# Kernel tuning notes

Measured on AMD Instinct MI355X. Metric: run time of the kernel, lower is better.

Reference implementation:

```python
import jax, jax.numpy as jnp
import numpy as np

INPUT_SIZE = 768
HIDDEN = 384


def _gru_dir(x, W_ih, W_hh, b_ih, b_hh, reverse):
    """Single-direction GRU, torch gate order (r, z, n).
    x: [B, S, D] -> outputs [B, S, H]."""
    B = x.shape[0]
    H = W_hh.shape[1]
    # Precompute input projections for all timesteps: [B, S, 3H] -> [S, B, 3H]
    xw = jnp.swapaxes(x @ W_ih.T + b_ih, 0, 1)

    def step(h, xw_t):
        gh = h @ W_hh.T + b_hh
        xr, xz, xn = jnp.split(xw_t, 3, axis=-1)
        hr, hz, hn = jnp.split(gh, 3, axis=-1)
        r = jax.nn.sigmoid(xr + hr)
        z = jax.nn.sigmoid(xz + hz)
        n = jnp.tanh(xn + r * hn)
        h_new = (1.0 - z) * n + z * h
        return h_new, h_new

    h0 = jnp.zeros((B, H), dtype=x.dtype)
    _, hs = jax.lax.scan(step, h0, xw, reverse=reverse)  # [S, B, H]
    return jnp.swapaxes(hs, 0, 1)


def setup_inputs() -> dict:
    key = jax.random.key(0)
    ks = jax.random.split(key, 12)
    B, S, D, H = 32, 512, INPUT_SIZE, HIDDEN
    s_ih = 1.0 / np.sqrt(H)
    u = lambda k, shape: jax.random.uniform(k, shape, jnp.float32, -s_ih, s_ih)
    inp = {
        "ip": jax.random.normal(ks[0], (B, S, D), jnp.float32),
        # forward-direction GRU params
        "W_ih_f": u(ks[1], (3 * H, D)),
        "W_hh_f": u(ks[2], (3 * H, H)),
        "b_ih_f": u(ks[3], (3 * H,)),
        "b_hh_f": u(ks[4], (3 * H,)),
        # backward-direction GRU params
        "W_ih_b": u(ks[5], (3 * H, D)),
        "W_hh_b": u(ks[6], (3 * H, H)),
        "b_ih_b": u(ks[7], (3 * H,)),
        "b_hh_b": u(ks[8], (3 * H,)),
        # sentence attention params (input_dim = 2H)
        "W_attn": u(ks[9], (2 * H, 2 * H)),
        "b_attn": u(ks[10], (2 * H,)),
        "context": jax.random.normal(ks[11], (2 * H,), jnp.float32) * 0.05,
    }
    return inp


def reference(ip, W_ih_f, W_hh_f, b_ih_f, b_hh_f,
              W_ih_b, W_hh_b, b_ih_b, b_hh_b,
              W_attn, b_attn, context):
    # BiGRU encode: concat forward & backward hidden states -> [B, S, 2H]
    h_f = _gru_dir(ip, W_ih_f, W_hh_f, b_ih_f, b_hh_f, reverse=False)
    h_b = _gru_dir(ip, W_ih_b, W_hh_b, b_ih_b, b_hh_b, reverse=True)
    out = jnp.concatenate([h_f, h_b], axis=-1)
    # Additive attention pooling over sentences
    scores = jnp.tanh(out @ W_attn.T + b_attn) @ context  # [B, S]
    attn = jax.nn.softmax(scores, axis=1)
    doc_embeds = jnp.einsum("bs,bsd->bd", attn, out)  # [B, 2H]
    return doc_embeds
```

## Files before the change

kernel.cpp:

```cpp
#include <hip/hip_runtime.h>
#include <hip/hip_fp16.h>

typedef _Float16 half2_t __attribute__((ext_vector_type(2)));
typedef _Float16 half4_t __attribute__((ext_vector_type(4)));
typedef _Float16 half8_t __attribute__((ext_vector_type(8)));
typedef float floatx4 __attribute__((ext_vector_type(4)));

#define B_   32
#define S_   512
#define D_   768
#define H_   384
#define H3_  1152
#define M_   (B_*S_)
#define N2_  (2*H3_)
#define TWOH_ 768
#define NWG_DIR 6
#define JSPAN 64

__device__ __forceinline__ void load16_cc3(const void* p0, const void* p1, const void* p2,
                                           int4& v0, int4& v1, int4& v2) {
  unsigned long long a0 = (unsigned long long)p0;
  unsigned long long a1 = (unsigned long long)p1;
  unsigned long long a2 = (unsigned long long)p2;
  asm volatile("global_load_dwordx4 %0, %3, off sc1\n\t"
               "global_load_dwordx4 %1, %4, off sc1\n\t"
               "global_load_dwordx4 %2, %5, off sc1\n\t"
               "s_waitcnt vmcnt(0)"
               : "=&v"(v0), "=&v"(v1), "=&v"(v2)
               : "v"(a0), "v"(a1), "v"(a2) : "memory");
}
__device__ __forceinline__ void store8_cc(void* p, int2 v) {
  unsigned long long a = (unsigned long long)p;
  asm volatile("global_store_dwordx2 %0, %1, off sc1" :: "v"(a), "v"(v) : "memory");
}
__device__ __forceinline__ void wait_vm0() {
  asm volatile("s_waitcnt vmcnt(0)" ::: "memory");
}

__global__ void cvt_f32_f16_kernel(const float* __restrict__ src,
                                   _Float16* __restrict__ dst, int n4) {
  int i = blockIdx.x * blockDim.x + threadIdx.x;
  if (i >= n4) return;
  float4 v = ((const float4*)src)[i];
  half4_t h = {(_Float16)v.x, (_Float16)v.y, (_Float16)v.z, (_Float16)v.w};
  ((half4_t*)dst)[i] = h;
}

__global__ __launch_bounds__(256) void gemm_xw_kernel(
    const _Float16* __restrict__ A, const _Float16* __restrict__ Bm,
    const float* __restrict__ bias_f, const float* __restrict__ bias_b,
    _Float16* __restrict__ xw) {
  __shared__ _Float16 As[64][40];
  __shared__ _Float16 Bs[64][40];
  const int m0 = blockIdx.x * 64, n0 = blockIdx.y * 64;
  const int tid = threadIdx.x, lane = tid & 63, w = tid >> 6;
  const int wm = w >> 1, wn = w & 1;
  const int q = lane >> 4, c = lane & 15;
  floatx4 acc[2][2] = {};

  const int t = tid & 127;
  const int srow = t >> 1, skh = (t & 1) * 16;
  const _Float16* gsrc =
      (tid < 128 ? A + (size_t)(m0 + srow) * D_ : Bm + (size_t)(n0 + srow) * D_) + skh;
  _Float16* ldst = (tid < 128) ? &As[srow][skh] : &Bs[srow][skh];

  for (int k0 = 0; k0 < D_; k0 += 32) {
    half8_t v0 = *(const half8_t*)(gsrc + k0);
    half8_t v1 = *(const half8_t*)(gsrc + k0 + 8);
    __syncthreads();
    *(half8_t*)ldst = v0;
    *(half8_t*)(ldst + 8) = v1;
    __syncthreads();
    half8_t a0 = *(const half8_t*)&As[wm * 32 + c][q * 8];
    half8_t a1 = *(const half8_t*)&As[wm * 32 + 16 + c][q * 8];
    half8_t b0 = *(const half8_t*)&Bs[wn * 32 + c][q * 8];
    half8_t b1 = *(const half8_t*)&Bs[wn * 32 + 16 + c][q * 8];
    acc[0][0] = __builtin_amdgcn_mfma_f32_16x16x32_f16(a0, b0, acc[0][0], 0, 0, 0);
    acc[0][1] = __builtin_amdgcn_mfma_f32_16x16x32_f16(a0, b1, acc[0][1], 0, 0, 0);
    acc[1][0] = __builtin_amdgcn_mfma_f32_16x16x32_f16(a1, b0, acc[1][0], 0, 0, 0);
    acc[1][1] = __builtin_amdgcn_mfma_f32_16x16x32_f16(a1, b1, acc[1][1], 0, 0, 0);
  }
  for (int mi = 0; mi < 2; ++mi)
    for (int ni = 0; ni < 2; ++ni)
      for (int r = 0; r < 4; ++r) {
        int m = m0 + wm * 32 + mi * 16 + q * 4 + r;
        int n = n0 + wn * 32 + ni * 16 + c;
        int dir = n >= H3_;
        int nn = n - dir * H3_;
        float bv = dir ? bias_b[nn] : bias_f[nn];
        float vv = acc[mi][ni][r] + bv;
        int s = m & (S_ - 1), bb = m >> 9;
        xw[(((size_t)dir * S_ + s) * B_ + bb) * H3_ + nn] = (_Float16)vv;
      }
}

__global__ __launch_bounds__(512, 2) void gru_mfma_kernel(
    const _Float16* __restrict__ xw,
    const _Float16* __restrict__ Whh,
    const float* __restrict__ bhh_f, const float* __restrict__ bhh_b,
    _Float16* __restrict__ hglob,
    _Float16* __restrict__ out16,
    int* __restrict__ bar) {
  const int wg = blockIdx.x;
  const int dir = wg / NWG_DIR;
  const int wgj = wg % NWG_DIR;
  const int j0w = wgj * JSPAN;
  const int tid = threadIdx.x, lane = tid & 63, w = tid >> 6;
  const int bt = w & 1, jt = w >> 1;
  const int c = lane & 15, q = lane >> 4;

  __shared__ __align__(16) _Float16 hS[32 * 392];

  half8_t bfr[3][12];
  {
    const int jglob = j0w + jt * 16 + c;
#pragma unroll
    for (int g = 0; g < 3; ++g) {
      const _Float16* wp = Whh + ((size_t)dir * H3_ + g * H_ + jglob) * H_ + q * 8;
#pragma unroll
      for (int kt = 0; kt < 12; ++kt) bfr[g][kt] = *(const half8_t*)(wp + kt * 32);
    }
  }
  const float* bhh = dir ? bhh_b : bhh_f;
  const int bl = bt * 16 + c;
  const int jg4 = j0w + jt * 16 + q * 4;
  const float4 br4 = *(const float4*)&bhh[jg4];
  const float4 bz4 = *(const float4*)&bhh[H_ + jg4];
  const float4 bn4 = *(const float4*)&bhh[2 * H_ + jg4];
  float hc[4] = {0.f, 0.f, 0.f, 0.f};

  int* flg = bar + dir * 256;

  for (int step = 0; step < S_; ++step) {
    const int t = dir ? (S_ - 1 - step) : step;
    const int par = step & 1;

    const _Float16* xbase = xw + (((size_t)dir * S_ + t) * B_ + bl) * H3_ + jg4;
    half4_t xr4 = *(const half4_t*)(xbase);
    half4_t xz4 = *(const half4_t*)(xbase + H_);
    half4_t xn4 = *(const half4_t*)(xbase + 2 * H_);

    if (step > 0 && w == 0) {
      int v;
      do {
        v = (lane < NWG_DIR)
                ? __hip_atomic_load(&flg[lane * 16], __ATOMIC_RELAXED,
                                    __HIP_MEMORY_SCOPE_AGENT)
                : 0x7fffffff;
      } while (!__all(v >= step));
    }
    __syncthreads();

    {
      const _Float16* hb = hglob + ((size_t)dir * 2 + par) * B_ * H_;
      int g0 = tid, g1 = tid + 512, g2 = tid + 1024;
      int4 v0, v1, v2;
      load16_cc3(hb + (g0 / 48) * H_ + (g0 % 48) * 8,
                 hb + (g1 / 48) * H_ + (g1 % 48) * 8,
                 hb + (g2 / 48) * H_ + (g2 % 48) * 8, v0, v1, v2);
      *(int4*)&hS[(g0 / 48) * 392 + (g0 % 48) * 8] = v0;
      *(int4*)&hS[(g1 / 48) * 392 + (g1 % 48) * 8] = v1;
      *(int4*)&hS[(g2 / 48) * 392 + (g2 % 48) * 8] = v2;
    }
    __syncthreads();

    floatx4 a0 = {}, a1 = {}, a2 = {};
    {
      const _Float16* hrow = &hS[(bt * 16 + c) * 392 + q * 8];
#pragma unroll
      for (int kt = 0; kt < 12; ++kt) {
        half8_t hf = *(const half8_t*)(hrow + kt * 32);
        a0 = __builtin_amdgcn_mfma_f32_16x16x32_f16(bfr[0][kt], hf, a0, 0, 0, 0);
        a1 = __builtin_amdgcn_mfma_f32_16x16x32_f16(bfr[1][kt], hf, a1, 0, 0, 0);
        a2 = __builtin_amdgcn_mfma_f32_16x16x32_f16(bfr[2][kt], hf, a2, 0, 0, 0);
      }
    }

    half4_t hh;
#pragma unroll
    for (int r = 0; r < 4; ++r) {
      float rr = 1.f / (1.f + __expf(-((float)xr4[r] + a0[r] + br4[r])));
      float zz = 1.f / (1.f + __expf(-((float)xz4[r] + a1[r] + bz4[r])));
      float u = (float)xn4[r] + rr * (a2[r] + bn4[r]);
      float e = __expf(-2.f * u);
      float nv = (1.f - e) / (1.f + e);
      hc[r] = (1.f - zz) * nv + zz * hc[r];
      hh[r] = (_Float16)hc[r];
    }
    store8_cc(hglob + (((size_t)dir * 2 + (par ^ 1)) * B_ + bl) * H_ + jg4,
              __builtin_bit_cast(int2, hh));
    wait_vm0();
    __syncthreads();
    if (tid == 0)
      __hip_atomic_store(&flg[wgj * 16], step + 1, __ATOMIC_RELAXED,
                         __HIP_MEMORY_SCOPE_AGENT);
    *(half4_t*)&out16[((size_t)bl * S_ + t) * TWOH_ + dir * H_ + jg4] = hh;
  }
}

__global__ __launch_bounds__(256) void attn_score_kernel(
    const _Float16* __restrict__ A ,
    const _Float16* __restrict__ Bm ,
    const float* __restrict__ b_attn, const float* __restrict__ ctx,
    float* __restrict__ scores) {
  __shared__ _Float16 As[64][40];
  __shared__ _Float16 Bs[64][40];
  const int m0 = blockIdx.x * 64, n0 = blockIdx.y * 64;
  const int tid = threadIdx.x, lane = tid & 63, w = tid >> 6;
  const int wm = w >> 1, wn = w & 1;
  const int q = lane >> 4, c = lane & 15;
  floatx4 acc[2][2] = {};

  const int t = tid & 127;
  const int srow = t >> 1, skh = (t & 1) * 16;
  const _Float16* gsrc =
      (tid < 128 ? A + (size_t)(m0 + srow) * D_ : Bm + (size_t)(n0 + srow) * D_) + skh;
  _Float16* ldst = (tid < 128) ? &As[srow][skh] : &Bs[srow][skh];

  for (int k0 = 0; k0 < D_; k0 += 32) {
    half8_t v0 = *(const half8_t*)(gsrc + k0);
    half8_t v1 = *(const half8_t*)(gsrc + k0 + 8);
    __syncthreads();
    *(half8_t*)ldst = v0;
    *(half8_t*)(ldst + 8) = v1;
    __syncthreads();
    half8_t a0 = *(const half8_t*)&As[wm * 32 + c][q * 8];
    half8_t a1 = *(const half8_t*)&As[wm * 32 + 16 + c][q * 8];
    half8_t b0 = *(const half8_t*)&Bs[wn * 32 + c][q * 8];
    half8_t b1 = *(const half8_t*)&Bs[wn * 32 + 16 + c][q * 8];
    acc[0][0] = __builtin_amdgcn_mfma_f32_16x16x32_f16(a0, b0, acc[0][0], 0, 0, 0);
    acc[0][1] = __builtin_amdgcn_mfma_f32_16x16x32_f16(a0, b1, acc[0][1], 0, 0, 0);
    acc[1][0] = __builtin_amdgcn_mfma_f32_16x16x32_f16(a1, b0, acc[1][0], 0, 0, 0);
    acc[1][1] = __builtin_amdgcn_mfma_f32_16x16x32_f16(a1, b1, acc[1][1], 0, 0, 0);
  }
  for (int mi = 0; mi < 2; ++mi)
    for (int ni = 0; ni < 2; ++ni)
      for (int r = 0; r < 4; ++r) {
        int n = n0 + wn * 32 + ni * 16 + c;
        float vv = tanhf(acc[mi][ni][r] + b_attn[n]) * ctx[n];
        vv += __shfl_xor(vv, 1);
        vv += __shfl_xor(vv, 2);
        vv += __shfl_xor(vv, 4);
        vv += __shfl_xor(vv, 8);
        if (c == 0) {
          int m = m0 + wm * 32 + mi * 16 + q * 4 + r;
          atomicAdd(&scores[m], vv);
        }
      }
}

__global__ __launch_bounds__(256) void softmax_kernel(const float* __restrict__ scores,
                                                      float* __restrict__ attn) {
  const int b = blockIdx.x, tid = threadIdx.x;
  __shared__ float red[8];
  float s0 = scores[b * S_ + tid], s1 = scores[b * S_ + 256 + tid];
  float m = fmaxf(s0, s1);
  for (int off = 1; off < 64; off <<= 1) m = fmaxf(m, __shfl_xor(m, off));
  int wv = tid >> 6;
  if ((tid & 63) == 0) red[wv] = m;
  __syncthreads();
  m = fmaxf(fmaxf(red[0], red[1]), fmaxf(red[2], red[3]));
  float e0 = expf(s0 - m), e1 = expf(s1 - m);
  float sum = e0 + e1;
  for (int off = 1; off < 64; off <<= 1) sum += __shfl_xor(sum, off);
  if ((tid & 63) == 0) red[4 + wv] = sum;
  __syncthreads();
  sum = red[4] + red[5] + red[6] + red[7];
  float inv = 1.0f / sum;
  attn[b * S_ + tid] = e0 * inv;
  attn[b * S_ + 256 + tid] = e1 * inv;
}

__global__ __launch_bounds__(384) void doc_kernel(const float* __restrict__ attn,
                                                  const _Float16* __restrict__ out16,
                                                  float* __restrict__ dout) {
  const int b = blockIdx.x, tid = threadIdx.x;
  __shared__ float at[S_];
  for (int i = tid; i < S_; i += 384) at[i] = attn[b * S_ + i];
  __syncthreads();
  const half2_t* p = (const half2_t*)(out16 + (size_t)b * S_ * TWOH_) + tid;
  float acc0 = 0.f, acc1 = 0.f;
  for (int s = 0; s < S_; ++s) {
    half2_t h = p[(size_t)s * (TWOH_ / 2)];
    float wgt = at[s];
    acc0 += wgt * (float)h.x;
    acc1 += wgt * (float)h.y;
  }
  dout[b * TWOH_ + tid * 2] = acc0;
  dout[b * TWOH_ + tid * 2 + 1] = acc1;
}

extern "C" void kernel_launch(void* const* d_in, const int* in_sizes, int n_in,
                              void* d_out, int out_size, void* d_ws, size_t ws_size,
                              hipStream_t stream) {
  const float* ip     = (const float*)d_in[0];
  const float* W_ih_f = (const float*)d_in[1];
  const float* W_hh_f = (const float*)d_in[2];
  const float* b_ih_f = (const float*)d_in[3];
  const float* b_hh_f_p = (const float*)d_in[4];
  const float* W_ih_b = (const float*)d_in[5];
  const float* W_hh_b = (const float*)d_in[6];
  const float* b_ih_b = (const float*)d_in[7];
  const float* b_hh_b_p = (const float*)d_in[8];
  const float* W_attn = (const float*)d_in[9];
  const float* b_attn = (const float*)d_in[10];
  const float* context = (const float*)d_in[11];
  float* doc = (float*)d_out;

  char* ws = (char*)d_ws;
  size_t off = 0;
  auto alloc = [&](size_t bytes) {
    char* p = ws + off;
    off += (bytes + 255) & ~(size_t)255;
    return p;
  };
  _Float16* ip16    = (_Float16*)alloc((size_t)M_ * D_ * 2);
  _Float16* Wih16   = (_Float16*)alloc((size_t)N2_ * D_ * 2);
  _Float16* Whh16   = (_Float16*)alloc((size_t)2 * H3_ * H_ * 2);
  _Float16* Wattn16 = (_Float16*)alloc((size_t)TWOH_ * TWOH_ * 2);
  _Float16* xw      = (_Float16*)alloc((size_t)2 * S_ * B_ * H3_ * 2);
  _Float16* out16   = (_Float16*)alloc((size_t)B_ * S_ * TWOH_ * 2);
  _Float16* hglob   = (_Float16*)alloc((size_t)2 * 2 * B_ * H_ * 2);
  int*      bar     = (int*)alloc(4096);
  float* scores     = (float*)alloc((size_t)M_ * 4);
  float* attn       = (float*)alloc((size_t)M_ * 4);

  cvt_f32_f16_kernel<<<(M_ * D_ / 4 + 255) / 256, 256, 0, stream>>>(ip, ip16, M_ * D_ / 4);
  cvt_f32_f16_kernel<<<(H3_ * D_ / 4 + 255) / 256, 256, 0, stream>>>(W_ih_f, Wih16, H3_ * D_ / 4);
  cvt_f32_f16_kernel<<<(H3_ * D_ / 4 + 255) / 256, 256, 0, stream>>>(W_ih_b, Wih16 + (size_t)H3_ * D_, H3_ * D_ / 4);
  cvt_f32_f16_kernel<<<(H3_ * H_ / 4 + 255) / 256, 256, 0, stream>>>(W_hh_f, Whh16, H3_ * H_ / 4);
  cvt_f32_f16_kernel<<<(H3_ * H_ / 4 + 255) / 256, 256, 0, stream>>>(W_hh_b, Whh16 + (size_t)H3_ * H_, H3_ * H_ / 4);
  cvt_f32_f16_kernel<<<(TWOH_ * TWOH_ / 4 + 255) / 256, 256, 0, stream>>>(W_attn, Wattn16, TWOH_ * TWOH_ / 4);

  gemm_xw_kernel<<<dim3(M_ / 64, N2_ / 64), 256, 0, stream>>>(ip16, Wih16, b_ih_f, b_ih_b, xw);

  hipMemsetAsync(hglob, 0, (size_t)2 * 2 * B_ * H_ * 2, stream);
  hipMemsetAsync(bar, 0, 4096, stream);
  {
    const _Float16* xw_a = xw;
    const _Float16* whh_a = Whh16;
    const float* bf_a = b_hh_f_p;
    const float* bb_a = b_hh_b_p;
    _Float16* hg_a = hglob;
    _Float16* o16_a = out16;
    int* bar_a = bar;
    void* args[] = {(void*)&xw_a, (void*)&whh_a, (void*)&bf_a, (void*)&bb_a,
                    (void*)&hg_a, (void*)&o16_a, (void*)&bar_a};
    hipLaunchCooperativeKernel((const void*)gru_mfma_kernel, dim3(2 * NWG_DIR),
                               dim3(512), args, 0, stream);
  }

  hipMemsetAsync(scores, 0, (size_t)M_ * 4, stream);
  attn_score_kernel<<<dim3(M_ / 64, TWOH_ / 64), 256, 0, stream>>>(out16, Wattn16, b_attn, context, scores);

  softmax_kernel<<<B_, 256, 0, stream>>>(scores, attn);
  doc_kernel<<<B_, 384, 0, stream>>>(attn, out16, doc);
}
```

Measured before the change: 2.217 ms.

## Fuse input-projection GEMM into GRU kernel with worker blocks and readiness flags

Removes the separate xw GEMM launch. A single cooperative grid of 256 blocks now runs the 12 GRU recurrence blocks alongside 244 worker blocks. The workers compute 128x128 projection tiles in timestep-chunk order, so the early forward and backward chunks finish first, and each completed tile bumps a per-chunk readiness counter. GRU blocks wait on that counter before consuming a chunk, which lets the recurrence overlap most of the GEMM. The xw loads are also merged into the same asm gather as the h loads. The risks are extra spin-waiting, scattered 2-byte stores with the sc1 cache policy, and the GEMM tiles competing with the latency-critical GRU blocks for hardware resources.

```diff
diff --git a/kernel.cpp b/kernel.cpp
--- a/kernel.cpp
+++ b/kernel.cpp
@@ -16,25 +16,52 @@
 #define TWOH_ 768
 #define NWG_DIR 6
 #define JSPAN 64
-
-__device__ __forceinline__ void load16_cc3(const void* p0, const void* p1, const void* p2,
-                                           int4& v0, int4& v1, int4& v2) {
-  unsigned long long a0 = (unsigned long long)p0;
-  unsigned long long a1 = (unsigned long long)p1;
-  unsigned long long a2 = (unsigned long long)p2;
-  asm volatile("global_load_dwordx4 %0, %3, off sc1\n\t"
-               "global_load_dwordx4 %1, %4, off sc1\n\t"
-               "global_load_dwordx4 %2, %5, off sc1\n\t"
-               "s_waitcnt vmcnt(0)"
-               : "=&v"(v0), "=&v"(v1), "=&v"(v2)
-               : "v"(a0), "v"(a1), "v"(a2) : "memory");
-}
+#define GRID_ 256
+#define NGRU_ 12
+#define NWORK_ (GRID_ - NGRU_)
+#define NTILES_ 2304
+#define TPL_ 576
+#define XWTGT_ 288
+
 __device__ __forceinline__ void store8_cc(void* p, int2 v) {
   unsigned long long a = (unsigned long long)p;
   asm volatile("global_store_dwordx2 %0, %1, off sc1" :: "v"(a), "v"(v) : "memory");
 }
+__device__ __forceinline__ void store2_cc(void* p, unsigned short v) {
+  unsigned long long a = (unsigned long long)p;
+  unsigned d = v;
+  asm volatile("global_store_short %0, %1, off sc1" :: "v"(a), "v"(d) : "memory");
+}
 __device__ __forceinline__ void wait_vm0() {
   asm volatile("s_waitcnt vmcnt(0)" ::: "memory");
+}
+__device__ __forceinline__ void gather6(const void* p0, const void* p1, const void* p2,
+                                        const void* x0, const void* x1, const void* x2,
+                                        int4& v0, int4& v1, int4& v2,
+                                        int2& r0, int2& r1, int2& r2) {
+  asm volatile("global_load_dwordx4 %0, %6, off sc1\n\t"
+               "global_load_dwordx4 %1, %7, off sc1\n\t"
+               "global_load_dwordx4 %2, %8, off sc1\n\t"
+               "global_load_dwordx2 %3, %9, off sc1\n\t"
+               "global_load_dwordx2 %4, %10, off sc1\n\t"
+               "global_load_dwordx2 %5, %11, off sc1\n\t"
+               "s_waitcnt vmcnt(0)"
+               : "=&v"(v0), "=&v"(v1), "=&v"(v2), "=&v"(r0), "=&v"(r1), "=&v"(r2)
+               : "v"((unsigned long long)p0), "v"((unsigned long long)p1),
+                 "v"((unsigned long long)p2), "v"((unsigned long long)x0),
+                 "v"((unsigned long long)x1), "v"((unsigned long long)x2)
+               : "memory");
+}
+__device__ __forceinline__ void load_xw3(const void* x0, const void* x1, const void* x2,
+                                         int2& r0, int2& r1, int2& r2) {
+  asm volatile("global_load_dwordx2 %0, %3, off sc1\n\t"
+               "global_load_dwordx2 %1, %4, off sc1\n\t"
+               "global_load_dwordx2 %2, %5, off sc1\n\t"
+               "s_waitcnt vmcnt(0)"
+               : "=&v"(r0), "=&v"(r1), "=&v"(r2)
+               : "v"((unsigned long long)x0), "v"((unsigned long long)x1),
+                 "v"((unsigned long long)x2)
+               : "memory");
 }
 
 __global__ void cvt_f32_f16_kernel(const float* __restrict__ src,
@@ -46,70 +73,89 @@
   ((half4_t*)dst)[i] = h;
 }
 
-__global__ __launch_bounds__(256) void gemm_xw_kernel(
-    const _Float16* __restrict__ A, const _Float16* __restrict__ Bm,
-    const float* __restrict__ bias_f, const float* __restrict__ bias_b,
-    _Float16* __restrict__ xw) {
-  __shared__ _Float16 As[64][40];
-  __shared__ _Float16 Bs[64][40];
-  const int m0 = blockIdx.x * 64, n0 = blockIdx.y * 64;
-  const int tid = threadIdx.x, lane = tid & 63, w = tid >> 6;
-  const int wm = w >> 1, wn = w & 1;
-  const int q = lane >> 4, c = lane & 15;
-  floatx4 acc[2][2] = {};
-
-  const int t = tid & 127;
-  const int srow = t >> 1, skh = (t & 1) * 16;
-  const _Float16* gsrc =
-      (tid < 128 ? A + (size_t)(m0 + srow) * D_ : Bm + (size_t)(n0 + srow) * D_) + skh;
-  _Float16* ldst = (tid < 128) ? &As[srow][skh] : &Bs[srow][skh];
-
-  for (int k0 = 0; k0 < D_; k0 += 32) {
-    half8_t v0 = *(const half8_t*)(gsrc + k0);
-    half8_t v1 = *(const half8_t*)(gsrc + k0 + 8);
-    __syncthreads();
-    *(half8_t*)ldst = v0;
-    *(half8_t*)(ldst + 8) = v1;
-    __syncthreads();
-    half8_t a0 = *(const half8_t*)&As[wm * 32 + c][q * 8];
-    half8_t a1 = *(const half8_t*)&As[wm * 32 + 16 + c][q * 8];
-    half8_t b0 = *(const half8_t*)&Bs[wn * 32 + c][q * 8];
-    half8_t b1 = *(const half8_t*)&Bs[wn * 32 + 16 + c][q * 8];
-    acc[0][0] = __builtin_amdgcn_mfma_f32_16x16x32_f16(a0, b0, acc[0][0], 0, 0, 0);
-    acc[0][1] = __builtin_amdgcn_mfma_f32_16x16x32_f16(a0, b1, acc[0][1], 0, 0, 0);
-    acc[1][0] = __builtin_amdgcn_mfma_f32_16x16x32_f16(a1, b0, acc[1][0], 0, 0, 0);
-    acc[1][1] = __builtin_amdgcn_mfma_f32_16x16x32_f16(a1, b1, acc[1][1], 0, 0, 0);
-  }
-  for (int mi = 0; mi < 2; ++mi)
-    for (int ni = 0; ni < 2; ++ni)
-      for (int r = 0; r < 4; ++r) {
-        int m = m0 + wm * 32 + mi * 16 + q * 4 + r;
-        int n = n0 + wn * 32 + ni * 16 + c;
-        int dir = n >= H3_;
-        int nn = n - dir * H3_;
-        float bv = dir ? bias_b[nn] : bias_f[nn];
-        float vv = acc[mi][ni][r] + bv;
-        int s = m & (S_ - 1), bb = m >> 9;
-        xw[(((size_t)dir * S_ + s) * B_ + bb) * H3_ + nn] = (_Float16)vv;
-      }
-}
-
-__global__ __launch_bounds__(512, 2) void gru_mfma_kernel(
-    const _Float16* __restrict__ xw,
+__global__ __launch_bounds__(512, 2) void fused_kernel(
+    const _Float16* __restrict__ ip16,
+    const _Float16* __restrict__ Wih16,
+    const float* __restrict__ b_ih_f, const float* __restrict__ b_ih_b,
+    _Float16* __restrict__ xw,
     const _Float16* __restrict__ Whh,
     const float* __restrict__ bhh_f, const float* __restrict__ bhh_b,
     _Float16* __restrict__ hglob,
     _Float16* __restrict__ out16,
     int* __restrict__ bar) {
+  __shared__ __align__(16) _Float16 As[128][40];
+  __shared__ __align__(16) _Float16 Bs[128][40];
+  __shared__ __align__(16) _Float16 hS[32 * 392];
+
+  const int tid = threadIdx.x, lane = tid & 63, w = tid >> 6;
+  const int c = lane & 15, q = lane >> 4;
+  int* const ready = bar + 640;
+
+  if (blockIdx.x >= NGRU_) {
+    const int wid = blockIdx.x - NGRU_;
+    const int wm = w >> 1, wn = w & 1;
+    for (int g = wid; g < NTILES_; g += NWORK_) {
+      const int l = g / TPL_;
+      const int layer = (0x9C >> (2 * l)) & 3;
+      const int ww = g - l * TPL_;
+      const int b = ww / 18, nt = ww - b * 18;
+      const int m0 = b * 512 + layer * 128;
+      const int n0 = nt * 128;
+      const int dirt = nt >= 9;
+      floatx4 acc[2][4] = {};
+
+      const int srow = (tid & 255) >> 1, soff = (tid & 1) * 16;
+      const _Float16* gsrc =
+          (tid < 256 ? ip16 + (size_t)(m0 + srow) * D_
+                     : Wih16 + (size_t)(n0 + srow) * D_) + soff;
+      _Float16* ldst = (tid < 256) ? &As[srow][soff] : &Bs[srow][soff];
+
+      for (int k0 = 0; k0 < D_; k0 += 32) {
+        half8_t v0 = *(const half8_t*)(gsrc + k0);
+        half8_t v1 = *(const half8_t*)(gsrc + k0 + 8);
+        __syncthreads();
+        *(half8_t*)ldst = v0;
+        *(half8_t*)(ldst + 8) = v1;
+        __syncthreads();
+        half8_t a0 = *(const half8_t*)&As[wm * 32 + c][q * 8];
+        half8_t a1 = *(const half8_t*)&As[wm * 32 + 16 + c][q * 8];
+#pragma unroll
+        for (int ni = 0; ni < 4; ++ni) {
+          half8_t bf = *(const half8_t*)&Bs[wn * 64 + ni * 16 + c][q * 8];
+          acc[0][ni] = __builtin_amdgcn_mfma_f32_16x16x32_f16(a0, bf, acc[0][ni], 0, 0, 0);
+          acc[1][ni] = __builtin_amdgcn_mfma_f32_16x16x32_f16(a1, bf, acc[1][ni], 0, 0, 0);
+        }
+      }
+#pragma unroll
+      for (int mi = 0; mi < 2; ++mi)
+#pragma unroll
+        for (int ni = 0; ni < 4; ++ni)
+#pragma unroll
+          for (int r = 0; r < 4; ++r) {
+            int m = m0 + wm * 32 + mi * 16 + q * 4 + r;
+            int n = n0 + wn * 64 + ni * 16 + c;
+            int nn = n - dirt * H3_;
+            float bv = dirt ? b_ih_b[nn] : b_ih_f[nn];
+            float vv = acc[mi][ni][r] + bv;
+            int s = m & (S_ - 1), bb = m >> 9;
+            _Float16 hv = (_Float16)vv;
+            store2_cc(&xw[(((size_t)dirt * S_ + s) * B_ + bb) * H3_ + nn],
+                      __builtin_bit_cast(unsigned short, hv));
+          }
+      wait_vm0();
+      __syncthreads();
+      if (tid == 0)
+        __hip_atomic_fetch_add(&ready[dirt * 4 + layer], 1, __ATOMIC_RELEASE,
+                               __HIP_MEMORY_SCOPE_AGENT);
+    }
+    return;
+  }
+
   const int wg = blockIdx.x;
   const int dir = wg / NWG_DIR;
   const int wgj = wg % NWG_DIR;
   const int j0w = wgj * JSPAN;
-  const int tid = threadIdx.x, lane = tid & 63, w = tid >> 6;
   const int bt = w & 1, jt = w >> 1;
-  const int c = lane & 15, q = lane >> 4;
-
-  __shared__ __align__(16) _Float16 hS[32 * 392];
 
   half8_t bfr[3][12];
   {
@@ -130,34 +176,46 @@
   float hc[4] = {0.f, 0.f, 0.f, 0.f};
 
   int* flg = bar + dir * 256;
+  int xwok = -1;
 
   for (int step = 0; step < S_; ++step) {
     const int t = dir ? (S_ - 1 - step) : step;
     const int par = step & 1;
 
+    const int cur128 = t >> 7;
+    if (cur128 != xwok) {
+      if (tid == 0) {
+        while (__hip_atomic_load(&ready[dir * 4 + cur128], __ATOMIC_ACQUIRE,
+                                 __HIP_MEMORY_SCOPE_AGENT) < XWTGT_) {}
+      }
+      __syncthreads();
+      xwok = cur128;
+    }
+
     const _Float16* xbase = xw + (((size_t)dir * S_ + t) * B_ + bl) * H3_ + jg4;
-    half4_t xr4 = *(const half4_t*)(xbase);
-    half4_t xz4 = *(const half4_t*)(xbase + H_);
-    half4_t xn4 = *(const half4_t*)(xbase + 2 * H_);
-
-    if (step > 0 && w == 0) {
-      int v;
-      do {
-        v = (lane < NWG_DIR)
-                ? __hip_atomic_load(&flg[lane * 16], __ATOMIC_RELAXED,
-                                    __HIP_MEMORY_SCOPE_AGENT)
-                : 0x7fffffff;
-      } while (!__all(v >= step));
-    }
-    __syncthreads();
-
-    {
+    int2 xri, xzi, xni;
+
+    if (step == 0) {
+      load_xw3(xbase, xbase + H_, xbase + 2 * H_, xri, xzi, xni);
+      for (int i = tid; i < 32 * 392 / 2; i += 512) ((int*)hS)[i] = 0;
+    } else {
+      if (w == 0) {
+        int v;
+        do {
+          v = (lane < NWG_DIR)
+                  ? __hip_atomic_load(&flg[lane * 16], __ATOMIC_RELAXED,
+                                      __HIP_MEMORY_SCOPE_AGENT)
+                  : 0x7fffffff;
+        } while (!__all(v >= step));
+      }
+      __syncthreads();
       const _Float16* hb = hglob + ((size_t)dir * 2 + par) * B_ * H_;
       int g0 = tid, g1 = tid + 512, g2 = tid + 1024;
       int4 v0, v1, v2;
-      load16_cc3(hb + (g0 / 48) * H_ + (g0 % 48) * 8,
-                 hb + (g1 / 48) * H_ + (g1 % 48) * 8,
-                 hb + (g2 / 48) * H_ + (g2 % 48) * 8, v0, v1, v2);
+      gather6(hb + (g0 / 48) * H_ + (g0 % 48) * 8,
+              hb + (g1 / 48) * H_ + (g1 % 48) * 8,
+              hb + (g2 / 48) * H_ + (g2 % 48) * 8,
+              xbase, xbase + H_, xbase + 2 * H_, v0, v1, v2, xri, xzi, xni);
       *(int4*)&hS[(g0 / 48) * 392 + (g0 % 48) * 8] = v0;
       *(int4*)&hS[(g1 / 48) * 392 + (g1 % 48) * 8] = v1;
       *(int4*)&hS[(g2 / 48) * 392 + (g2 % 48) * 8] = v2;
@@ -176,6 +234,9 @@
       }
     }
 
+    half4_t xr4 = __builtin_bit_cast(half4_t, xri);
+    half4_t xz4 = __builtin_bit_cast(half4_t, xzi);
+    half4_t xn4 = __builtin_bit_cast(half4_t, xni);
     half4_t hh;
 #pragma unroll
     for (int r = 0; r < 4; ++r) {
@@ -332,21 +393,24 @@
   cvt_f32_f16_kernel<<<(H3_ * H_ / 4 + 255) / 256, 256, 0, stream>>>(W_hh_b, Whh16 + (size_t)H3_ * H_, H3_ * H_ / 4);
   cvt_f32_f16_kernel<<<(TWOH_ * TWOH_ / 4 + 255) / 256, 256, 0, stream>>>(W_attn, Wattn16, TWOH_ * TWOH_ / 4);
 
-  gemm_xw_kernel<<<dim3(M_ / 64, N2_ / 64), 256, 0, stream>>>(ip16, Wih16, b_ih_f, b_ih_b, xw);
-
   hipMemsetAsync(hglob, 0, (size_t)2 * 2 * B_ * H_ * 2, stream);
   hipMemsetAsync(bar, 0, 4096, stream);
   {
-    const _Float16* xw_a = xw;
+    const _Float16* ip_a = ip16;
+    const _Float16* wih_a = Wih16;
+    const float* bif_a = b_ih_f;
+    const float* bib_a = b_ih_b;
+    _Float16* xw_a = xw;
     const _Float16* whh_a = Whh16;
     const float* bf_a = b_hh_f_p;
     const float* bb_a = b_hh_b_p;
     _Float16* hg_a = hglob;
     _Float16* o16_a = out16;
     int* bar_a = bar;
-    void* args[] = {(void*)&xw_a, (void*)&whh_a, (void*)&bf_a, (void*)&bb_a,
+    void* args[] = {(void*)&ip_a, (void*)&wih_a, (void*)&bif_a, (void*)&bib_a,
+                    (void*)&xw_a, (void*)&whh_a, (void*)&bf_a, (void*)&bb_a,
                     (void*)&hg_a, (void*)&o16_a, (void*)&bar_a};
-    hipLaunchCooperativeKernel((const void*)gru_mfma_kernel, dim3(2 * NWG_DIR),
+    hipLaunchCooperativeKernel((const void*)fused_kernel, dim3(GRID_),
                                dim3(512), args, 0, stream);
   }
 
```

Measured after the change: 2.428 ms. +9.5%, slower.
